# Kernel optimization log

Measured on AMD Instinct MI355X. Metric: run time of the kernel, lower is better.

Reference implementation:

```python
import jax, jax.numpy as jnp
import numpy as np

MUL = 64          # channel multiplicity per irrep
N_NODES = 50000
SQRT3 = float(np.sqrt(3.0))
SQRT6 = float(np.sqrt(6.0))
# e3nn-style path weights (path_normalization='element', irrep_normalization='component'):
# out 0e (dim 1) receives 2 paths -> sqrt(1/2); out 1e (dim 3) receives 3 paths -> sqrt(3/3)=1
PW0 = float(np.sqrt(1.0 / 2.0))
PW1 = 1.0


def _spherical_harmonics_l1(edge_vec):
    # normalize=True, normalization='component': Y0 = 1, Y1 = sqrt(3) * r_hat
    n = jnp.linalg.norm(edge_vec, axis=-1, keepdims=True)
    r = edge_vec / jnp.maximum(n, 1e-12)
    sh0 = jnp.ones(edge_vec.shape[:-1], edge_vec.dtype)  # [E]
    sh1 = SQRT3 * r                                      # [E,3]
    return sh0, sh1


def _forward(x, edge_vec, weight, edge_src, edge_dst):
    E = edge_vec.shape[0]
    sh0, sh1 = _spherical_harmonics_l1(edge_vec)
    # split node features: 64x0e | 64x1e
    x0 = x[:, :MUL]                         # [N, mul]
    x1 = x[:, MUL:].reshape(-1, MUL, 3)     # [N, mul, 3]
    xs0 = x0[edge_src]                      # [E, mul] gather
    xs1 = x1[edge_src]                      # [E, mul, 3]
    # per-edge weights, one mul-vector per uvu path, e3nn instruction order
    w = weight.reshape(E, 5, MUL)
    w000, w011, w101, w110, w111 = (w[:, i, :] for i in range(5))
    # Wigner-3j (Frobenius-normalized) contractions:
    # 0e x 0e -> 0e : C=1 ; 1e x 1e -> 0e : delta/sqrt(3)
    msg0 = PW0 * (w000 * xs0 * sh0[:, None]
                  + w110 * (jnp.einsum('euk,ek->eu', xs1, sh1) / SQRT3))  # [E, mul]
    # 0e x 1e -> 1e : delta/sqrt(3) ; 1e x 0e -> 1e : delta/sqrt(3) ; 1e x 1e -> 1e : eps/sqrt(6)
    cross = jnp.cross(xs1, sh1[:, None, :])  # [E, mul, 3], eps_ijk x_i s_j
    msg1 = PW1 * (w011[:, :, None] * xs0[:, :, None] * sh1[:, None, :] / SQRT3
                  + w101[:, :, None] * xs1 * (sh0[:, None, None] / SQRT3)
                  + w111[:, :, None] * cross / SQRT6)  # [E, mul, 3]
    msg = jnp.concatenate([msg0, msg1.reshape(E, MUL * 3)], axis=1)  # [E, 256]
    # scatter-sum over destination nodes
    return jax.ops.segment_sum(msg, edge_dst, num_segments=N_NODES)


def setup_inputs() -> dict:
    key = jax.random.key(0)
    k1, k2, k3, k4, k5 = jax.random.split(key, 5)
    E = 400000
    return {
        'x': jax.random.normal(k1, (N_NODES, 4 * MUL), dtype=jnp.float32),
        'edge_vec': jax.random.normal(k2, (E, 3), dtype=jnp.float32),
        'weight': jax.random.normal(k3, (E, 5 * MUL), dtype=jnp.float32),
        'edge_src': jax.random.randint(k4, (E,), 0, N_NODES, dtype=jnp.int64),
        'edge_dst': jax.random.randint(k5, (E,), 0, N_NODES, dtype=jnp.int64),
    }


def reference(x, edge_vec, weight, edge_src, edge_dst):
    return _forward(x, edge_vec, weight, edge_src, edge_dst)
```

## Files before the change

### kernel.cpp

```cpp
#include <hip/hip_runtime.h>

#define MUL 64
#define XROW 256
#define WROW 320

typedef int   i32x4 __attribute__((ext_vector_type(4)));
typedef float f32x4 __attribute__((ext_vector_type(4)));

struct __align__(32) Rec { int e, src; float rx, ry, rz; int p0, p1, p2; };


__global__ void k_xt_zero(const float* __restrict__ x, f32x4* __restrict__ xt,
                          int* __restrict__ counts, int N) {
    int t = blockIdx.x * blockDim.x + threadIdx.x;
    if (t < N) counts[t] = 0;
    if (t >= N * 64) return;
    const int n = t >> 6, u = t & 63;
    const float* xr = x + (size_t)n * XROW;
    f32x4 v;
    v.x = xr[u];
    v.y = xr[MUL + 3 * u + 0];
    v.z = xr[MUL + 3 * u + 1];
    v.w = xr[MUL + 3 * u + 2];
    xt[t] = v;
}

__global__ void k_hist(const int* __restrict__ dst, int* __restrict__ counts, int E) {
    int i = blockIdx.x * blockDim.x + threadIdx.x;
    if (i < E) atomicAdd(&counts[dst[i]], 1);
}

__global__ void k_scan1(const int* __restrict__ counts, int* __restrict__ offs,
                        int* __restrict__ bsums, int N) {
    __shared__ int s[256];
    int t = threadIdx.x;
    int i = blockIdx.x * 256 + t;
    int v = (i < N) ? counts[i] : 0;
    s[t] = v; __syncthreads();
    for (int off = 1; off < 256; off <<= 1) {
        int tmp = (t >= off) ? s[t - off] : 0;
        __syncthreads();
        s[t] += tmp;
        __syncthreads();
    }
    if (i < N) offs[i] = s[t] - v;
    if (t == 255) bsums[blockIdx.x] = s[255];
}

__global__ void k_scan2(int* __restrict__ bsums, int nb) {
    __shared__ int s[256];
    int t = threadIdx.x;
    int v = (t < nb) ? bsums[t] : 0;
    s[t] = v; __syncthreads();
    for (int off = 1; off < 256; off <<= 1) {
        int tmp = (t >= off) ? s[t - off] : 0;
        __syncthreads();
        s[t] += tmp;
        __syncthreads();
    }
    if (t < nb) bsums[t] = s[t] - v;
}

__global__ void k_scatter_pack(const int* __restrict__ dst, const int* __restrict__ src,
                               const float* __restrict__ ev,
                               const int* __restrict__ offs, const int* __restrict__ bsums,
                               int* __restrict__ counts, Rec* __restrict__ rec, int E) {
    int i = blockIdx.x * blockDim.x + threadIdx.x;
    if (i >= E) return;
    const int d = dst[i];
    const int pos = offs[d] + bsums[d >> 8] + (atomicSub(&counts[d], 1) - 1);
    const float ex = ev[3 * i + 0], ey = ev[3 * i + 1], ez = ev[3 * i + 2];
    const float rn = 1.0f / fmaxf(sqrtf(ex * ex + ey * ey + ez * ez), 1e-12f);
    Rec r;
    r.e = i; r.src = src[i];
    r.rx = ex * rn; r.ry = ey * rn; r.rz = ez * rn;
    r.p0 = 0; r.p1 = 0; r.p2 = 0;
    rec[pos] = r;
}


__global__ __launch_bounds__(256) void k_accum(
    const float* __restrict__ weight,
    const f32x4* __restrict__ xt,
    const Rec* __restrict__ rec,
    const int* __restrict__ offs,
    const int* __restrict__ bsums,
    float* __restrict__ out,
    int N, int E)
{
    const int wave = blockIdx.x * (blockDim.x >> 6) + (threadIdx.x >> 6);
    const int lane = threadIdx.x & 63;
    if (wave >= N) return;
    const int n = wave;
    const int start = offs[n] + bsums[n >> 8];
    const int end   = (n + 1 < N) ? (offs[n + 1] + bsums[(n + 1) >> 8]) : E;

    const float PW0       = 0.70710678118654752440f;
    const float INV_SQRT3 = 0.57735026918962576451f;
    const float INV_SQRT2 = 0.70710678118654752440f;

    float a0 = 0.f, a1x = 0.f, a1y = 0.f, a1z = 0.f;

    if (start < end) {
        const i32x4* ri = (const i32x4*)rec;
        const float* rf = (const float*)rec;
        const int last = end - 1;

        i32x4 h0  = __builtin_nontemporal_load(ri + 2 * start);
        float rz0 = __builtin_nontemporal_load(rf + 8 * start + 4);
        const int j1 = (start + 1 < last) ? start + 1 : last;
        i32x4 h1  = __builtin_nontemporal_load(ri + 2 * j1);
        float rz1 = __builtin_nontemporal_load(rf + 8 * j1 + 4);
        const float* w0p = weight + (size_t)h0.x * WROW;
        float w000 = __builtin_nontemporal_load(w0p + 0 * MUL + lane);
        float w011 = __builtin_nontemporal_load(w0p + 1 * MUL + lane);
        float w101 = __builtin_nontemporal_load(w0p + 2 * MUL + lane);
        float w110 = __builtin_nontemporal_load(w0p + 3 * MUL + lane);
        float w111 = __builtin_nontemporal_load(w0p + 4 * MUL + lane);
        f32x4 xv = xt[(size_t)h0.y * 64 + lane];

        for (int i = start; i < end; ++i) {
            const int j2 = (i + 2 < last) ? i + 2 : last;
            const i32x4 h2  = __builtin_nontemporal_load(ri + 2 * j2);
            const float rz2 = __builtin_nontemporal_load(rf + 8 * j2 + 4);

            const float* w1p = weight + (size_t)h1.x * WROW;
            const float nw000 = __builtin_nontemporal_load(w1p + 0 * MUL + lane);
            const float nw011 = __builtin_nontemporal_load(w1p + 1 * MUL + lane);
            const float nw101 = __builtin_nontemporal_load(w1p + 2 * MUL + lane);
            const float nw110 = __builtin_nontemporal_load(w1p + 3 * MUL + lane);
            const float nw111 = __builtin_nontemporal_load(w1p + 4 * MUL + lane);
            const f32x4 nxv = xt[(size_t)h1.y * 64 + lane];

            const float rx = __int_as_float(h0.z);
            const float ry = __int_as_float(h0.w);
            const float rz = rz0;

            const float dotv = xv.y * rx + xv.z * ry + xv.w * rz;
            a0 += PW0 * (w000 * xv.x + w110 * dotv);

            const float cx = xv.z * rz - xv.w * ry;
            const float cy = xv.w * rx - xv.y * rz;
            const float cz = xv.y * ry - xv.z * rx;

            const float a = w011 * xv.x;
            const float b = w101 * INV_SQRT3;
            const float c = w111 * INV_SQRT2;
            a1x += a * rx + b * xv.y + c * cx;
            a1y += a * ry + b * xv.z + c * cy;
            a1z += a * rz + b * xv.w + c * cz;

            h0 = h1; rz0 = rz1;
            h1 = h2; rz1 = rz2;
            w000 = nw000; w011 = nw011; w101 = nw101; w110 = nw110; w111 = nw111;
            xv = nxv;
        }
    }

    float* o = out + (size_t)n * XROW;
    __builtin_nontemporal_store(a0,  o + lane);
    __builtin_nontemporal_store(a1x, o + MUL + 3 * lane + 0);
    __builtin_nontemporal_store(a1y, o + MUL + 3 * lane + 1);
    __builtin_nontemporal_store(a1z, o + MUL + 3 * lane + 2);
}


__global__ __launch_bounds__(256) void tpconv_edge_kernel(
    const float* __restrict__ x, const float* __restrict__ edge_vec,
    const float* __restrict__ weight, const int* __restrict__ edge_src,
    const int* __restrict__ edge_dst, float* __restrict__ out, int E)
{
    const int wave = blockIdx.x * (blockDim.x >> 6) + (threadIdx.x >> 6);
    const int lane = threadIdx.x & 63;
    if (wave >= E) return;
    const int e = wave;
    const int src = edge_src[e];
    const int dst = edge_dst[e];
    const float evx = edge_vec[3 * e + 0], evy = edge_vec[3 * e + 1], evz = edge_vec[3 * e + 2];
    const float rn = 1.0f / fmaxf(sqrtf(evx * evx + evy * evy + evz * evz), 1e-12f);
    const float rx = evx * rn, ry = evy * rn, rz = evz * rn;
    const float* xr = x + (size_t)src * XROW;
    const float xs0 = xr[lane];
    const float x1x = xr[MUL + 3 * lane + 0], x1y = xr[MUL + 3 * lane + 1], x1z = xr[MUL + 3 * lane + 2];
    const float* w = weight + (size_t)e * WROW;
    const float w000 = w[lane], w011 = w[MUL + lane], w101 = w[2 * MUL + lane],
                w110 = w[3 * MUL + lane], w111 = w[4 * MUL + lane];
    const float PW0 = 0.70710678118654752440f, INV_SQRT3 = 0.57735026918962576451f,
                INV_SQRT2 = 0.70710678118654752440f;
    const float dotv = x1x * rx + x1y * ry + x1z * rz;
    const float m0 = PW0 * (w000 * xs0 + w110 * dotv);
    const float cx = x1y * rz - x1z * ry, cy = x1z * rx - x1x * rz, cz = x1x * ry - x1y * rx;
    const float a = w011 * xs0, b = w101 * INV_SQRT3, c = w111 * INV_SQRT2;
    float* o = out + (size_t)dst * XROW;
    atomicAdd(o + lane, m0);
    atomicAdd(o + MUL + 3 * lane + 0, a * rx + b * x1x + c * cx);
    atomicAdd(o + MUL + 3 * lane + 1, a * ry + b * x1y + c * cy);
    atomicAdd(o + MUL + 3 * lane + 2, a * rz + b * x1z + c * cz);
}

extern "C" void kernel_launch(void* const* d_in, const int* in_sizes, int n_in,
                              void* d_out, int out_size, void* d_ws, size_t ws_size,
                              hipStream_t stream) {
    const float* x        = (const float*)d_in[0];
    const float* edge_vec = (const float*)d_in[1];
    const float* weight   = (const float*)d_in[2];
    const int*   edge_src = (const int*)d_in[3];
    const int*   edge_dst = (const int*)d_in[4];
    float* out = (float*)d_out;

    const int E = in_sizes[3];
    const int N = in_sizes[0] / XROW;
    const int nb1 = (N + 255) / 256;

    int*  counts = (int*)d_ws;
    int*  offs   = counts + N;
    int*  bsums  = offs + N;
    Rec*  recb   = (Rec*)(bsums + 256);
    f32x4* xtb   = (f32x4*)((char*)recb + (size_t)E * sizeof(Rec));
    const size_t need = (size_t)(2 * N + 256) * 4 + (size_t)E * sizeof(Rec)
                      + (size_t)N * 64 * sizeof(f32x4);

    if (ws_size < need || nb1 > 256) {
        (void)hipMemsetAsync(d_out, 0, (size_t)out_size * sizeof(float), stream);
        tpconv_edge_kernel<<<(E + 3) / 4, 256, 0, stream>>>(
            x, edge_vec, weight, edge_src, edge_dst, out, E);
        return;
    }

    k_xt_zero<<<(N * 64 + 255) / 256, 256, 0, stream>>>(x, xtb, counts, N);
    k_hist<<<(E + 255) / 256, 256, 0, stream>>>(edge_dst, counts, E);
    k_scan1<<<nb1, 256, 0, stream>>>(counts, offs, bsums, N);
    k_scan2<<<1, 256, 0, stream>>>(bsums, nb1);
    k_scatter_pack<<<(E + 255) / 256, 256, 0, stream>>>(
        edge_dst, edge_src, edge_vec, offs, bsums, counts, recb, E);
    k_accum<<<(N + 3) / 4, 256, 0, stream>>>(
        weight, xtb, recb, offs, bsums, out, N, E);
}
```

Before: 207.5 us.

## Replace CSR sort with fixed-capacity per-node buckets and atomic overflow path

Drops the histogram and two-level scan kernels. Edges are now written straight into fixed-capacity (96-slot) per-destination buckets using an atomic slot counter, and any edge past capacity goes to an overflow list that a small atomic-add kernel handles afterwards. The accumulate kernel reads counts instead of offsets, and its software prefetch is deepened from two to three edges ahead. This removes three kernel launches and a pass over edge_dst. In exchange the record buffer is much larger and sparsely filled, and the wider prefetch raises register use.

```diff
diff --git a/kernel.cpp b/kernel.cpp
--- a/kernel.cpp
+++ b/kernel.cpp
@@ -3,6 +3,7 @@
 #define MUL 64
 #define XROW 256
 #define WROW 320
+#define CAP  96
 
 typedef int   i32x4 __attribute__((ext_vector_type(4)));
 typedef float f32x4 __attribute__((ext_vector_type(4)));
@@ -11,9 +12,10 @@
 
 
 __global__ void k_xt_zero(const float* __restrict__ x, f32x4* __restrict__ xt,
-                          int* __restrict__ counts, int N) {
+                          int* __restrict__ counts, int* __restrict__ ovfcnt, int N) {
     int t = blockIdx.x * blockDim.x + threadIdx.x;
     if (t < N) counts[t] = 0;
+    if (t == 0) *ovfcnt = 0;
     if (t >= N * 64) return;
     const int n = t >> 6, u = t & 63;
     const float* xr = x + (size_t)n * XROW;
@@ -25,57 +27,27 @@
     xt[t] = v;
 }
 
-__global__ void k_hist(const int* __restrict__ dst, int* __restrict__ counts, int E) {
-    int i = blockIdx.x * blockDim.x + threadIdx.x;
-    if (i < E) atomicAdd(&counts[dst[i]], 1);
-}
-
-__global__ void k_scan1(const int* __restrict__ counts, int* __restrict__ offs,
-                        int* __restrict__ bsums, int N) {
-    __shared__ int s[256];
-    int t = threadIdx.x;
-    int i = blockIdx.x * 256 + t;
-    int v = (i < N) ? counts[i] : 0;
-    s[t] = v; __syncthreads();
-    for (int off = 1; off < 256; off <<= 1) {
-        int tmp = (t >= off) ? s[t - off] : 0;
-        __syncthreads();
-        s[t] += tmp;
-        __syncthreads();
-    }
-    if (i < N) offs[i] = s[t] - v;
-    if (t == 255) bsums[blockIdx.x] = s[255];
-}
-
-__global__ void k_scan2(int* __restrict__ bsums, int nb) {
-    __shared__ int s[256];
-    int t = threadIdx.x;
-    int v = (t < nb) ? bsums[t] : 0;
-    s[t] = v; __syncthreads();
-    for (int off = 1; off < 256; off <<= 1) {
-        int tmp = (t >= off) ? s[t - off] : 0;
-        __syncthreads();
-        s[t] += tmp;
-        __syncthreads();
-    }
-    if (t < nb) bsums[t] = s[t] - v;
-}
 
 __global__ void k_scatter_pack(const int* __restrict__ dst, const int* __restrict__ src,
                                const float* __restrict__ ev,
-                               const int* __restrict__ offs, const int* __restrict__ bsums,
-                               int* __restrict__ counts, Rec* __restrict__ rec, int E) {
+                               int* __restrict__ counts, Rec* __restrict__ rec,
+                               int* __restrict__ ovf, int* __restrict__ ovfcnt, int E) {
     int i = blockIdx.x * blockDim.x + threadIdx.x;
     if (i >= E) return;
     const int d = dst[i];
-    const int pos = offs[d] + bsums[d >> 8] + (atomicSub(&counts[d], 1) - 1);
+    const int slot = atomicAdd(&counts[d], 1);
+    if (slot >= CAP) {
+        int oi = atomicAdd(ovfcnt, 1);
+        ovf[oi] = i;
+        return;
+    }
     const float ex = ev[3 * i + 0], ey = ev[3 * i + 1], ez = ev[3 * i + 2];
     const float rn = 1.0f / fmaxf(sqrtf(ex * ex + ey * ey + ez * ez), 1e-12f);
     Rec r;
     r.e = i; r.src = src[i];
     r.rx = ex * rn; r.ry = ey * rn; r.rz = ez * rn;
     r.p0 = 0; r.p1 = 0; r.p2 = 0;
-    rec[pos] = r;
+    rec[(size_t)d * CAP + slot] = r;
 }
 
 
@@ -83,17 +55,15 @@
     const float* __restrict__ weight,
     const f32x4* __restrict__ xt,
     const Rec* __restrict__ rec,
-    const int* __restrict__ offs,
-    const int* __restrict__ bsums,
+    const int* __restrict__ counts,
     float* __restrict__ out,
-    int N, int E)
+    int N)
 {
     const int wave = blockIdx.x * (blockDim.x >> 6) + (threadIdx.x >> 6);
     const int lane = threadIdx.x & 63;
     if (wave >= N) return;
-    const int n = wave;
-    const int start = offs[n] + bsums[n >> 8];
-    const int end   = (n + 1 < N) ? (offs[n + 1] + bsums[(n + 1) >> 8]) : E;
+    const int n   = wave;
+    const int cnt = min(counts[n], CAP);
 
     const float PW0       = 0.70710678118654752440f;
     const float INV_SQRT3 = 0.57735026918962576451f;
@@ -101,16 +71,21 @@
 
     float a0 = 0.f, a1x = 0.f, a1y = 0.f, a1z = 0.f;
 
-    if (start < end) {
+    if (cnt > 0) {
+        const size_t base = (size_t)n * CAP;
         const i32x4* ri = (const i32x4*)rec;
         const float* rf = (const float*)rec;
-        const int last = end - 1;
-
-        i32x4 h0  = __builtin_nontemporal_load(ri + 2 * start);
-        float rz0 = __builtin_nontemporal_load(rf + 8 * start + 4);
-        const int j1 = (start + 1 < last) ? start + 1 : last;
-        i32x4 h1  = __builtin_nontemporal_load(ri + 2 * j1);
-        float rz1 = __builtin_nontemporal_load(rf + 8 * j1 + 4);
+        const int last = cnt - 1;
+
+        i32x4 h0  = ri[2 * (base + 0)];
+        float rz0 = rf[8 * (base + 0) + 4];
+        const int j1 = (1 < last) ? 1 : last;
+        i32x4 h1  = ri[2 * (base + j1)];
+        float rz1 = rf[8 * (base + j1) + 4];
+        const int j2p = (2 < last) ? 2 : last;
+        i32x4 h2  = ri[2 * (base + j2p)];
+        float rz2 = rf[8 * (base + j2p) + 4];
+
         const float* w0p = weight + (size_t)h0.x * WROW;
         float w000 = __builtin_nontemporal_load(w0p + 0 * MUL + lane);
         float w011 = __builtin_nontemporal_load(w0p + 1 * MUL + lane);
@@ -119,18 +94,26 @@
         float w111 = __builtin_nontemporal_load(w0p + 4 * MUL + lane);
         f32x4 xv = xt[(size_t)h0.y * 64 + lane];
 
-        for (int i = start; i < end; ++i) {
-            const int j2 = (i + 2 < last) ? i + 2 : last;
-            const i32x4 h2  = __builtin_nontemporal_load(ri + 2 * j2);
-            const float rz2 = __builtin_nontemporal_load(rf + 8 * j2 + 4);
-
-            const float* w1p = weight + (size_t)h1.x * WROW;
-            const float nw000 = __builtin_nontemporal_load(w1p + 0 * MUL + lane);
-            const float nw011 = __builtin_nontemporal_load(w1p + 1 * MUL + lane);
-            const float nw101 = __builtin_nontemporal_load(w1p + 2 * MUL + lane);
-            const float nw110 = __builtin_nontemporal_load(w1p + 3 * MUL + lane);
-            const float nw111 = __builtin_nontemporal_load(w1p + 4 * MUL + lane);
-            const f32x4 nxv = xt[(size_t)h1.y * 64 + lane];
+        const float* w1p = weight + (size_t)h1.x * WROW;
+        float v000 = __builtin_nontemporal_load(w1p + 0 * MUL + lane);
+        float v011 = __builtin_nontemporal_load(w1p + 1 * MUL + lane);
+        float v101 = __builtin_nontemporal_load(w1p + 2 * MUL + lane);
+        float v110 = __builtin_nontemporal_load(w1p + 3 * MUL + lane);
+        float v111 = __builtin_nontemporal_load(w1p + 4 * MUL + lane);
+        f32x4 yv = xt[(size_t)h1.y * 64 + lane];
+
+        for (int i = 0; i < cnt; ++i) {
+            const int j3 = (i + 3 < last) ? i + 3 : last;
+            const i32x4 h3  = ri[2 * (base + j3)];
+            const float rz3 = rf[8 * (base + j3) + 4];
+
+            const float* w2p = weight + (size_t)h2.x * WROW;
+            const float u000 = __builtin_nontemporal_load(w2p + 0 * MUL + lane);
+            const float u011 = __builtin_nontemporal_load(w2p + 1 * MUL + lane);
+            const float u101 = __builtin_nontemporal_load(w2p + 2 * MUL + lane);
+            const float u110 = __builtin_nontemporal_load(w2p + 3 * MUL + lane);
+            const float u111 = __builtin_nontemporal_load(w2p + 4 * MUL + lane);
+            const f32x4 zv = xt[(size_t)h2.y * 64 + lane];
 
             const float rx = __int_as_float(h0.z);
             const float ry = __int_as_float(h0.w);
@@ -152,8 +135,11 @@
 
             h0 = h1; rz0 = rz1;
             h1 = h2; rz1 = rz2;
-            w000 = nw000; w011 = nw011; w101 = nw101; w110 = nw110; w111 = nw111;
-            xv = nxv;
+            h2 = h3; rz2 = rz3;
+            w000 = v000; w011 = v011; w101 = v101; w110 = v110; w111 = v111;
+            xv = yv;
+            v000 = u000; v011 = u011; v101 = u101; v110 = u110; v111 = u111;
+            yv = zv;
         }
     }
 
@@ -162,6 +148,42 @@
     __builtin_nontemporal_store(a1x, o + MUL + 3 * lane + 0);
     __builtin_nontemporal_store(a1y, o + MUL + 3 * lane + 1);
     __builtin_nontemporal_store(a1z, o + MUL + 3 * lane + 2);
+}
+
+
+__global__ void k_overflow(const float* __restrict__ weight, const f32x4* __restrict__ xt,
+                           const float* __restrict__ ev, const int* __restrict__ src,
+                           const int* __restrict__ dst,
+                           const int* __restrict__ ovf, const int* __restrict__ ovfcnt,
+                           float* __restrict__ out) {
+    const int nov = *ovfcnt;
+    const int wid  = blockIdx.x * (blockDim.x >> 6) + (threadIdx.x >> 6);
+    const int lane = threadIdx.x & 63;
+    const int nw   = gridDim.x * (blockDim.x >> 6);
+    const float PW0 = 0.70710678118654752440f, INV_SQRT3 = 0.57735026918962576451f,
+                INV_SQRT2 = 0.70710678118654752440f;
+    for (int k = wid; k < nov; k += nw) {
+        const int e = ovf[k];
+        const int s = src[e], d = dst[e];
+        const float ex = ev[3 * e + 0], ey = ev[3 * e + 1], ez = ev[3 * e + 2];
+        const float rn = 1.0f / fmaxf(sqrtf(ex * ex + ey * ey + ez * ez), 1e-12f);
+        const float rx = ex * rn, ry = ey * rn, rz = ez * rn;
+        const f32x4 xv = xt[(size_t)s * 64 + lane];
+        const float* w = weight + (size_t)e * WROW;
+        const float w000 = w[lane], w011 = w[MUL + lane], w101 = w[2 * MUL + lane],
+                    w110 = w[3 * MUL + lane], w111 = w[4 * MUL + lane];
+        const float dotv = xv.y * rx + xv.z * ry + xv.w * rz;
+        const float m0 = PW0 * (w000 * xv.x + w110 * dotv);
+        const float cx = xv.z * rz - xv.w * ry;
+        const float cy = xv.w * rx - xv.y * rz;
+        const float cz = xv.y * ry - xv.z * rx;
+        const float a = w011 * xv.x, b = w101 * INV_SQRT3, c = w111 * INV_SQRT2;
+        float* o = out + (size_t)d * XROW;
+        atomicAdd(o + lane, m0);
+        atomicAdd(o + MUL + 3 * lane + 0, a * rx + b * xv.y + c * cx);
+        atomicAdd(o + MUL + 3 * lane + 1, a * ry + b * xv.z + c * cy);
+        atomicAdd(o + MUL + 3 * lane + 2, a * rz + b * xv.w + c * cz);
+    }
 }
 
 
@@ -210,29 +232,27 @@
 
     const int E = in_sizes[3];
     const int N = in_sizes[0] / XROW;
-    const int nb1 = (N + 255) / 256;
 
     int*  counts = (int*)d_ws;
-    int*  offs   = counts + N;
-    int*  bsums  = offs + N;
-    Rec*  recb   = (Rec*)(bsums + 256);
-    f32x4* xtb   = (f32x4*)((char*)recb + (size_t)E * sizeof(Rec));
-    const size_t need = (size_t)(2 * N + 256) * 4 + (size_t)E * sizeof(Rec)
-                      + (size_t)N * 64 * sizeof(f32x4);
-
-    if (ws_size < need || nb1 > 256) {
+    int*  ovfcnt = counts + N;
+    int*  ovf    = ovfcnt + 8;
+    char* p      = (char*)(ovf + E);
+    p += (64 - ((size_t)p & 63)) & 63;
+    Rec*   recb  = (Rec*)p;
+    f32x4* xtb   = (f32x4*)((char*)recb + (size_t)N * CAP * sizeof(Rec));
+    const size_t need = ((char*)xtb + (size_t)N * 64 * sizeof(f32x4)) - (char*)d_ws;
+
+    if (ws_size < need) {
         (void)hipMemsetAsync(d_out, 0, (size_t)out_size * sizeof(float), stream);
         tpconv_edge_kernel<<<(E + 3) / 4, 256, 0, stream>>>(
             x, edge_vec, weight, edge_src, edge_dst, out, E);
         return;
     }
 
-    k_xt_zero<<<(N * 64 + 255) / 256, 256, 0, stream>>>(x, xtb, counts, N);
-    k_hist<<<(E + 255) / 256, 256, 0, stream>>>(edge_dst, counts, E);
-    k_scan1<<<nb1, 256, 0, stream>>>(counts, offs, bsums, N);
-    k_scan2<<<1, 256, 0, stream>>>(bsums, nb1);
+    k_xt_zero<<<(N * 64 + 255) / 256, 256, 0, stream>>>(x, xtb, counts, ovfcnt, N);
     k_scatter_pack<<<(E + 255) / 256, 256, 0, stream>>>(
-        edge_dst, edge_src, edge_vec, offs, bsums, counts, recb, E);
-    k_accum<<<(N + 3) / 4, 256, 0, stream>>>(
-        weight, xtb, recb, offs, bsums, out, N, E);
-}
+        edge_dst, edge_src, edge_vec, counts, recb, ovf, ovfcnt, E);
+    k_accum<<<(N + 3) / 4, 256, 0, stream>>>(weight, xtb, recb, counts, out, N);
+    k_overflow<<<16, 256, 0, stream>>>(weight, xtb, edge_vec, edge_src, edge_dst,
+                                       ovf, ovfcnt, out);
+}
```

Measured after the change: 181.7 us. 12.4% less time.
